# Kernel optimization log

Hardware: AMD Instinct MI355X
Metric: run time of the kernel (lower is better)

The kernel has to match this reference:

```python
import jax, jax.numpy as jnp
import numpy as np

B, S, IN, OUT = 4, 2048, 4096, 1024
ROUNDS = 12  # prime_factors(4096) == [2]*12
QMIN, QMAX = -128, 127


def _create_noise(key, shape, lo, hi):
    # Obfuscation noise spanning the data range; exactly corrected in forward.
    return jax.random.uniform(key, shape, jnp.float32, -0.5, 0.5) * (hi - lo)


def setup_inputs() -> dict:
    key = jax.random.key(0)
    ks = jax.random.split(key, 6)
    x = jax.random.normal(ks[0], (B, S, IN), jnp.float32)
    weight = jax.random.normal(ks[1], (OUT, IN), jnp.float32) * 0.02
    bias = jax.random.normal(ks[2], (OUT,), jnp.float32) * 0.02
    weight_noise = _create_noise(ks[3], (OUT, IN), weight.min(), weight.max())
    noise_x = _create_noise(ks[4], (B, S, IN), x.min(), x.max())
    # one random permutation of in_features per round
    perms = jnp.stack([jax.random.permutation(jax.random.fold_in(key, 1000 + r), IN)
                       for r in range(ROUNDS)]).astype(jnp.int32)
    # 2048 random orthogonal 2x2 blocks per round (rotations, like ortho_group with dim=2)
    theta = jax.random.uniform(ks[5], (ROUNDS, IN // 2), jnp.float32, 0.0, 2.0 * np.pi)
    c, s = jnp.cos(theta), jnp.sin(theta)
    row0 = jnp.stack([c, -s], axis=-1)
    row1 = jnp.stack([s, c], axis=-1)
    matrices = jnp.stack([row0, row1], axis=-2)  # (ROUNDS, IN//2, 2, 2)
    return {"x": x, "weight": weight, "bias": bias, "weight_noise": weight_noise,
            "noise_x": noise_x, "permutations": perms, "matrices": matrices}


def _permute_matrix_operation(X, perms, mats):
    # X: (..., n, cols). Each round: gather rows by permutation, then apply a
    # block-diagonal orthogonal transform (G blocks of size f along the n axis).
    lead = X.shape[:-2]
    n, cols = X.shape[-2], X.shape[-1]
    G, f = mats.shape[1], mats.shape[2]
    for r in range(mats.shape[0]):
        X = jnp.take(X, perms[r], axis=-2)
        Xb = X.reshape(lead + (G, f, cols))
        X = jnp.einsum('gij,...gjc->...gic', mats[r], Xb).reshape(lead + (n, cols))
    return X


def _quant_dequant(t):
    # Asymmetric per-tensor quantize -> round -> clamp -> dequantize (int8-style).
    lo, hi = t.min(), t.max()
    scale = (hi - lo) / (QMAX - QMIN)
    zp = jnp.round(QMIN - lo / scale)
    q = jnp.clip(jnp.round(t / scale + zp), QMIN, QMAX)
    return (q - zp) * scale


def reference(x, weight, bias, weight_noise, noise_x, permutations, matrices):
    # inverse-transpose blocks; equals `matrices` for orthogonal blocks, kept explicit for fidelity
    inv_mats_mT = jnp.swapaxes(jnp.linalg.inv(matrices), -1, -2)
    w_plus = weight + weight_noise                                   # (OUT, IN)
    permuted_w = jnp.swapaxes(
        _permute_matrix_operation(jnp.swapaxes(w_plus, -1, -2), permutations, inv_mats_mT), -1, -2)
    qw = _quant_dequant(permuted_w)                                  # (OUT, IN)
    permuted_x = jnp.swapaxes(
        _permute_matrix_operation(jnp.swapaxes(x + noise_x, -1, -2), permutations, matrices), -1, -2)
    qx = _quant_dequant(permuted_x)                                  # (B, S, IN)
    res = qx @ qw.T + bias                                           # quantized matmul + bias
    res = res - x @ weight_noise.T                                   # correction term 1
    res = res - noise_x @ w_plus.T                                   # correction term 2
    return res
```

## Files before the change

kernel.cpp:

```cpp
#include <hip/hip_runtime.h>


#define IN_F   4096
#define OUT_F  1024
#define MROWS  8192
#define KTOT   12288
#define NROUNDS 12

typedef _Float16 f16;
typedef _Float16 f16x8 __attribute__((ext_vector_type(8)));
typedef _Float16 f16x4 __attribute__((ext_vector_type(4)));
typedef float    f32x4 __attribute__((ext_vector_type(4)));

#define OFF_XT  (0ull)
#define OFF_WT  (OFF_XT + (size_t)MROWS * IN_F * 4)
#define OFF_A   (OFF_WT + (size_t)OUT_F * IN_F * 4)
#define OFF_B   (OFF_A + (size_t)MROWS * KTOT * 2)
#define OFF_MM  (OFF_B + (size_t)OUT_F * KTOT * 2)

__device__ __forceinline__ unsigned enc_f(float f) {
  unsigned u = __float_as_uint(f);
  return (u & 0x80000000u) ? ~u : (u | 0x80000000u);
}
__device__ __forceinline__ float dec_f(unsigned u) {
  unsigned b = (u & 0x80000000u) ? (u & 0x7fffffffu) : ~u;
  return __uint_as_float(b);
}

__global__ void init_mm_kernel(unsigned* mm) {
  mm[0] = 0xFFFFFFFFu;
  mm[1] = 0u;
  mm[2] = 0xFFFFFFFFu;
  mm[3] = 0u;
}

template <bool IS_W>
__global__ __launch_bounds__(256) void transform_kernel(
    const float* __restrict__ in0, const float* __restrict__ in1,
    const int* __restrict__ perms, const float* __restrict__ mats,
    float* __restrict__ tout, f16* __restrict__ f16out,
    unsigned* __restrict__ mm, int mmidx) {
  __shared__ float2 buf[2][IN_F];
  const int t = threadIdx.x;
  const size_t m0 = (size_t)blockIdx.x * 2;

  const float4* r0a = (const float4*)(in0 + m0 * IN_F);
  const float4* r0b = (const float4*)(in1 + m0 * IN_F);
  const float4* r1a = (const float4*)(in0 + (m0 + 1) * IN_F);
  const float4* r1b = (const float4*)(in1 + (m0 + 1) * IN_F);
  f16* f0 = f16out + m0 * KTOT;
  f16* f1 = f16out + (m0 + 1) * KTOT;

#pragma unroll
  for (int j = 0; j < 4; j++) {
    int i4 = j * 256 + t;
    float4 a0 = r0a[i4], b0 = r0b[i4], a1 = r1a[i4], b1 = r1b[i4];
    float4 s0 = make_float4(a0.x + b0.x, a0.y + b0.y, a0.z + b0.z, a0.w + b0.w);
    float4 s1 = make_float4(a1.x + b1.x, a1.y + b1.y, a1.z + b1.z, a1.w + b1.w);
    int c = i4 * 4;
    *(float4*)&buf[0][c]     = make_float4(s0.x, s1.x, s0.y, s1.y);
    *(float4*)&buf[0][c + 2] = make_float4(s0.z, s1.z, s0.w, s1.w);
    f16x4 p0, p1, q0, q1;
    if (IS_W) {
      p0.x=(f16)b0.x; p0.y=(f16)b0.y; p0.z=(f16)b0.z; p0.w=(f16)b0.w;
      q0.x=(f16)s0.x; q0.y=(f16)s0.y; q0.z=(f16)s0.z; q0.w=(f16)s0.w;
      p1.x=(f16)b1.x; p1.y=(f16)b1.y; p1.z=(f16)b1.z; p1.w=(f16)b1.w;
      q1.x=(f16)s1.x; q1.y=(f16)s1.y; q1.z=(f16)s1.z; q1.w=(f16)s1.w;
    } else {
      p0.x=(f16)(-a0.x); p0.y=(f16)(-a0.y); p0.z=(f16)(-a0.z); p0.w=(f16)(-a0.w);
      q0.x=(f16)(-b0.x); q0.y=(f16)(-b0.y); q0.z=(f16)(-b0.z); q0.w=(f16)(-b0.w);
      p1.x=(f16)(-a1.x); p1.y=(f16)(-a1.y); p1.z=(f16)(-a1.z); p1.w=(f16)(-a1.w);
      q1.x=(f16)(-b1.x); q1.y=(f16)(-b1.y); q1.z=(f16)(-b1.z); q1.w=(f16)(-b1.w);
    }
    *(f16x4*)(f0 + IN_F + c)     = p0;
    *(f16x4*)(f0 + 2 * IN_F + c) = q0;
    *(f16x4*)(f1 + IN_F + c)     = p1;
    *(f16x4*)(f1 + 2 * IN_F + c) = q1;
  }
  __syncthreads();

  int cur = 0;
  for (int r = 0; r < NROUNDS; r++) {
    const int2* prow = (const int2*)(perms + (size_t)r * IN_F);
    const float4* mrow = (const float4*)(mats + (size_t)r * (IN_F / 2) * 4);
#pragma unroll
    for (int i = 0; i < 8; i++) {
      int g = i * 256 + t;
      int2 p = prow[g];
      float4 m = mrow[g];
      float2 X0 = buf[cur][p.x];
      float2 X1 = buf[cur][p.y];
      float y0x, y0y, y1x, y1y;
      if (IS_W) {
        float rd = 1.0f / (m.x * m.w - m.y * m.z);
        y0x = (m.w * X0.x - m.z * X1.x) * rd;
        y0y = (m.w * X0.y - m.z * X1.y) * rd;
        y1x = (m.x * X1.x - m.y * X0.x) * rd;
        y1y = (m.x * X1.y - m.y * X0.y) * rd;
      } else {
        y0x = m.x * X0.x + m.y * X1.x;
        y0y = m.x * X0.y + m.y * X1.y;
        y1x = m.z * X0.x + m.w * X1.x;
        y1y = m.z * X0.y + m.w * X1.y;
      }
      *(float4*)&buf[cur ^ 1][2 * g] = make_float4(y0x, y0y, y1x, y1y);
    }
    cur ^= 1;
    __syncthreads();
  }
  float lmin = 3.4e38f, lmax = -3.4e38f;
  float4* o0 = (float4*)(tout + m0 * IN_F);
  float4* o1 = (float4*)(tout + (m0 + 1) * IN_F);
#pragma unroll
  for (int j = 0; j < 4; j++) {
    int i4 = j * 256 + t;
    int c = i4 * 4;
    float4 q0 = *(float4*)&buf[0][c];
    float4 q1 = *(float4*)&buf[0][c + 2];
    o0[i4] = make_float4(q0.x, q0.z, q1.x, q1.z);
    o1[i4] = make_float4(q0.y, q0.w, q1.y, q1.w);
    lmin = fminf(lmin, fminf(fminf(q0.x, q0.y), fminf(q0.z, q0.w)));
    lmin = fminf(lmin, fminf(fminf(q1.x, q1.y), fminf(q1.z, q1.w)));
    lmax = fmaxf(lmax, fmaxf(fmaxf(q0.x, q0.y), fmaxf(q0.z, q0.w)));
    lmax = fmaxf(lmax, fmaxf(fmaxf(q1.x, q1.y), fmaxf(q1.z, q1.w)));
  }
#pragma unroll
  for (int off = 32; off > 0; off >>= 1) {
    lmin = fminf(lmin, __shfl_down(lmin, off));
    lmax = fmaxf(lmax, __shfl_down(lmax, off));
  }
  float* red = (float*)&buf[1][0];
  int wid = t >> 6;
  if ((t & 63) == 0) { red[wid * 2] = lmin; red[wid * 2 + 1] = lmax; }
  __syncthreads();
  if (t == 0) {
    float bmin = fminf(fminf(red[0], red[2]), fminf(red[4], red[6]));
    float bmax = fmaxf(fmaxf(red[1], red[3]), fmaxf(red[5], red[7]));
    atomicMin(&mm[mmidx], enc_f(bmin));
    atomicMax(&mm[mmidx + 1], enc_f(bmax));
  }
}

__global__ void finalize_kernel(unsigned* mm) {
  float* sc = (float*)(mm + 4);
  float xlo = dec_f(mm[0]), xhi = dec_f(mm[1]);
  float wlo = dec_f(mm[2]), whi = dec_f(mm[3]);
  float sx = (xhi - xlo) / 255.0f;
  float zx = rintf(-128.0f - xlo / sx);
  float sw = (whi - wlo) / 255.0f;
  float zw = rintf(-128.0f - wlo / sw);
  sc[0] = sx; sc[1] = zx; sc[2] = sw; sc[3] = zw;
}

__global__ __launch_bounds__(256) void quant_kernel(
    const float* __restrict__ src, f16* __restrict__ dst,
    const unsigned* __restrict__ mm, int scoff) {
  const float* sc = (const float*)(mm + 4);
  float s = sc[scoff], zp = sc[scoff + 1];
  int m = blockIdx.x, t = threadIdx.x;
  const float4* srow = (const float4*)(src + (size_t)m * IN_F);
  f16* drow = dst + (size_t)m * KTOT;
#pragma unroll
  for (int j = 0; j < 4; j++) {
    int i4 = j * 256 + t;
    float4 v = srow[i4];
    float q0 = (fminf(fmaxf(rintf(v.x / s + zp), -128.f), 127.f) - zp) * s;
    float q1 = (fminf(fmaxf(rintf(v.y / s + zp), -128.f), 127.f) - zp) * s;
    float q2 = (fminf(fmaxf(rintf(v.z / s + zp), -128.f), 127.f) - zp) * s;
    float q3 = (fminf(fmaxf(rintf(v.w / s + zp), -128.f), 127.f) - zp) * s;
    f16x4 o; o.x = (f16)q0; o.y = (f16)q1; o.z = (f16)q2; o.w = (f16)q3;
    *(f16x4*)(drow + i4 * 4) = o;
  }
}

__device__ __forceinline__ void gl2lds16(const void* g, void* l) {
  __builtin_amdgcn_global_load_lds(
      (__attribute__((address_space(1))) void*)g,
      (__attribute__((address_space(3))) void*)l, 16, 0, 0);
}

__global__ __launch_bounds__(256, 2) void gemm_kernel(
    const f16* __restrict__ A, const f16* __restrict__ B,
    const float* __restrict__ bias, float* __restrict__ out) {
  __shared__ f16 As[128 * 32];
  __shared__ f16 Bs[128 * 32];
  const int tid = threadIdx.x;
  const int wave = tid >> 6, lane = tid & 63;
  const int quad = lane >> 4, fr = lane & 15;
  const int bm = blockIdx.x >> 3, bn = blockIdx.x & 7;
  const int wm = (wave & 1) * 64, wn = (wave >> 1) * 64;

  f32x4 acc[4][4] = {};

  const int l4 = lane >> 2;
  const int lc = (lane & 3) * 8;
  const size_t arow = (size_t)(bm * 128 + wave * 16 + l4);
  const size_t brow = (size_t)(bn * 128 + wave * 16 + l4);
  const f16* ag0 = A + arow * KTOT + lc;
  const f16* ag1 = A + (arow + 64) * KTOT + lc;
  const f16* bg0 = B + brow * KTOT + lc;
  const f16* bg1 = B + (brow + 64) * KTOT + lc;
  f16* as0 = As + (wave * 16) * 32;
  f16* as1 = As + (64 + wave * 16) * 32;
  f16* bs0 = Bs + (wave * 16) * 32;
  f16* bs1 = Bs + (64 + wave * 16) * 32;

  for (int kk = 0; kk < KTOT; kk += 32) {
    gl2lds16(ag0 + kk, as0);
    gl2lds16(ag1 + kk, as1);
    gl2lds16(bg0 + kk, bs0);
    gl2lds16(bg1 + kk, bs1);
    __syncthreads();
    f16x8 af[4], bf[4];
#pragma unroll
    for (int mi = 0; mi < 4; mi++)
      af[mi] = *(const f16x8*)(As + (wm + mi * 16 + fr) * 32 + quad * 8);
#pragma unroll
    for (int ni = 0; ni < 4; ni++)
      bf[ni] = *(const f16x8*)(Bs + (wn + ni * 16 + fr) * 32 + quad * 8);
#pragma unroll
    for (int mi = 0; mi < 4; mi++)
#pragma unroll
      for (int ni = 0; ni < 4; ni++)
        acc[mi][ni] = __builtin_amdgcn_mfma_f32_16x16x32_f16(
            af[mi], bf[ni], acc[mi][ni], 0, 0, 0);
    __syncthreads();
  }

#pragma unroll
  for (int mi = 0; mi < 4; mi++) {
    int gm = bm * 128 + wm + mi * 16 + quad * 4;
#pragma unroll
    for (int ni = 0; ni < 4; ni++) {
      int gn = bn * 128 + wn + ni * 16 + fr;
      float bv = bias[gn];
#pragma unroll
      for (int e = 0; e < 4; e++)
        out[(size_t)(gm + e) * OUT_F + gn] = acc[mi][ni][e] + bv;
    }
  }
}

extern "C" void kernel_launch(void* const* d_in, const int* in_sizes, int n_in,
                              void* d_out, int out_size, void* d_ws, size_t ws_size,
                              hipStream_t stream) {
  const float* x     = (const float*)d_in[0];
  const float* w     = (const float*)d_in[1];
  const float* bias  = (const float*)d_in[2];
  const float* wn    = (const float*)d_in[3];
  const float* nx    = (const float*)d_in[4];
  const int*   perms = (const int*)d_in[5];
  const float* mats  = (const float*)d_in[6];
  float* out = (float*)d_out;

  char* ws = (char*)d_ws;
  float* xt   = (float*)(ws + OFF_XT);
  float* wt   = (float*)(ws + OFF_WT);
  f16*   Aall = (f16*)(ws + OFF_A);
  f16*   Ball = (f16*)(ws + OFF_B);
  unsigned* mm = (unsigned*)(ws + OFF_MM);

  init_mm_kernel<<<1, 1, 0, stream>>>(mm);
  transform_kernel<false><<<MROWS / 2, 256, 0, stream>>>(x, nx, perms, mats, xt, Aall, mm, 0);
  transform_kernel<true><<<OUT_F / 2, 256, 0, stream>>>(w, wn, perms, mats, wt, Ball, mm, 2);
  finalize_kernel<<<1, 1, 0, stream>>>(mm);
  quant_kernel<<<MROWS, 256, 0, stream>>>(xt, Aall, mm, 0);
  quant_kernel<<<OUT_F, 256, 0, stream>>>(wt, Ball, mm, 2);
  gemm_kernel<<<(MROWS / 128) * (OUT_F / 128), 256, 0, stream>>>(Aall, Ball, bias, out);
}
```

Measured before the change: 821.7 us.

## Fuse pairs of permute-rotate rounds into precomputed 4-tap tables

A small kernel precomputes, for each pair of rounds, composed gather indices and combined 2x4 coefficients, including the inverse-transpose for the weight path. The transform kernel then runs 6 passes instead of 12, halving LDS round-trips and barriers at the cost of 4 gathers per output pair instead of 2. The GEMM block mapping is also changed so consecutive blocks walk along M for a fixed N tile, changing L2 reuse of the B operand. The fused coefficients are computed in fp32, so rounding differs slightly from the sequential rounds.

```diff
diff --git a/kernel.cpp b/kernel.cpp
--- a/kernel.cpp
+++ b/kernel.cpp
@@ -6,6 +6,7 @@
 #define MROWS  8192
 #define KTOT   12288
 #define NROUNDS 12
+#define NPASS  6
 
 typedef _Float16 f16;
 typedef _Float16 f16x8 __attribute__((ext_vector_type(8)));
@@ -17,6 +18,10 @@
 #define OFF_A   (OFF_WT + (size_t)OUT_F * IN_F * 4)
 #define OFF_B   (OFF_A + (size_t)MROWS * KTOT * 2)
 #define OFF_MM  (OFF_B + (size_t)OUT_F * KTOT * 2)
+#define OFF_TIX (OFF_MM + 256)
+#define OFF_TCX (OFF_TIX + (size_t)NPASS * 2048 * 16)
+#define OFF_TIW (OFF_TCX + (size_t)NPASS * 2048 * 32)
+#define OFF_TCW (OFF_TIW + (size_t)NPASS * 2048 * 16)
 
 __device__ __forceinline__ unsigned enc_f(float f) {
   unsigned u = __float_as_uint(f);
@@ -34,10 +39,50 @@
   mm[3] = 0u;
 }
 
+__global__ void build_tables_kernel(const int* __restrict__ perms,
+                                    const float* __restrict__ mats,
+                                    int4* __restrict__ tIx, float4* __restrict__ tCx,
+                                    int4* __restrict__ tIw, float4* __restrict__ tCw) {
+  int p = blockIdx.x;
+  int r0 = 2 * p, r1 = 2 * p + 1;
+  for (int g = threadIdx.x; g < 2048; g += blockDim.x) {
+    int q0 = perms[r1 * IN_F + 2 * g], q1 = perms[r1 * IN_F + 2 * g + 1];
+    int a0 = q0 >> 1, e0 = q0 & 1, a1 = q1 >> 1, e1 = q1 & 1;
+    int4 idx = make_int4(perms[r0 * IN_F + 2 * a0], perms[r0 * IN_F + 2 * a0 + 1],
+                         perms[r0 * IN_F + 2 * a1], perms[r0 * IN_F + 2 * a1 + 1]);
+    const float* Ma = mats + ((size_t)r0 * 2048 + a0) * 4;
+    const float* Mb = mats + ((size_t)r0 * 2048 + a1) * 4;
+    const float* M1 = mats + ((size_t)r1 * 2048 + g) * 4;
+    int o = p * 2048 + g;
+    {
+      float c00 = Ma[e0 * 2], c01 = Ma[e0 * 2 + 1];
+      float c10 = Mb[e1 * 2], c11 = Mb[e1 * 2 + 1];
+      float m00 = M1[0], m01 = M1[1], m10 = M1[2], m11 = M1[3];
+      tIx[o] = idx;
+      tCx[2 * o]     = make_float4(m00 * c00, m00 * c01, m01 * c10, m01 * c11);
+      tCx[2 * o + 1] = make_float4(m10 * c00, m10 * c01, m11 * c10, m11 * c11);
+    }
+    {
+      float rda = 1.0f / (Ma[0] * Ma[3] - Ma[1] * Ma[2]);
+      float rdb = 1.0f / (Mb[0] * Mb[3] - Mb[1] * Mb[2]);
+      float rd1 = 1.0f / (M1[0] * M1[3] - M1[1] * M1[2]);
+      float c00 = (e0 == 0 ? Ma[3] : -Ma[1]) * rda;
+      float c01 = (e0 == 0 ? -Ma[2] : Ma[0]) * rda;
+      float c10 = (e1 == 0 ? Mb[3] : -Mb[1]) * rdb;
+      float c11 = (e1 == 0 ? -Mb[2] : Mb[0]) * rdb;
+      float m00 = M1[3] * rd1, m01 = -M1[2] * rd1;
+      float m10 = -M1[1] * rd1, m11 = M1[0] * rd1;
+      tIw[o] = idx;
+      tCw[2 * o]     = make_float4(m00 * c00, m00 * c01, m01 * c10, m01 * c11);
+      tCw[2 * o + 1] = make_float4(m10 * c00, m10 * c01, m11 * c10, m11 * c11);
+    }
+  }
+}
+
 template <bool IS_W>
 __global__ __launch_bounds__(256) void transform_kernel(
     const float* __restrict__ in0, const float* __restrict__ in1,
-    const int* __restrict__ perms, const float* __restrict__ mats,
+    const int4* __restrict__ tI, const float4* __restrict__ tC,
     float* __restrict__ tout, f16* __restrict__ f16out,
     unsigned* __restrict__ mm, int mmidx) {
   __shared__ float2 buf[2][IN_F];
@@ -80,29 +125,20 @@
   __syncthreads();
 
   int cur = 0;
-  for (int r = 0; r < NROUNDS; r++) {
-    const int2* prow = (const int2*)(perms + (size_t)r * IN_F);
-    const float4* mrow = (const float4*)(mats + (size_t)r * (IN_F / 2) * 4);
+  for (int pass = 0; pass < NPASS; pass++) {
+    const int4* ti = tI + pass * 2048;
+    const float4* tc = tC + (size_t)pass * 4096;
 #pragma unroll
     for (int i = 0; i < 8; i++) {
       int g = i * 256 + t;
-      int2 p = prow[g];
-      float4 m = mrow[g];
-      float2 X0 = buf[cur][p.x];
-      float2 X1 = buf[cur][p.y];
-      float y0x, y0y, y1x, y1y;
-      if (IS_W) {
-        float rd = 1.0f / (m.x * m.w - m.y * m.z);
-        y0x = (m.w * X0.x - m.z * X1.x) * rd;
-        y0y = (m.w * X0.y - m.z * X1.y) * rd;
-        y1x = (m.x * X1.x - m.y * X0.x) * rd;
-        y1y = (m.x * X1.y - m.y * X0.y) * rd;
-      } else {
-        y0x = m.x * X0.x + m.y * X1.x;
-        y0y = m.x * X0.y + m.y * X1.y;
-        y1x = m.z * X0.x + m.w * X1.x;
-        y1y = m.z * X0.y + m.w * X1.y;
-      }
+      int4 id = ti[g];
+      float4 cA = tc[2 * g], cB = tc[2 * g + 1];
+      float2 x0 = buf[cur][id.x], x1 = buf[cur][id.y];
+      float2 x2 = buf[cur][id.z], x3 = buf[cur][id.w];
+      float y0x = cA.x * x0.x + cA.y * x1.x + cA.z * x2.x + cA.w * x3.x;
+      float y0y = cA.x * x0.y + cA.y * x1.y + cA.z * x2.y + cA.w * x3.y;
+      float y1x = cB.x * x0.x + cB.y * x1.x + cB.z * x2.x + cB.w * x3.x;
+      float y1y = cB.x * x0.y + cB.y * x1.y + cB.z * x2.y + cB.w * x3.y;
       *(float4*)&buf[cur ^ 1][2 * g] = make_float4(y0x, y0y, y1x, y1y);
     }
     cur ^= 1;
@@ -187,7 +223,7 @@
   const int tid = threadIdx.x;
   const int wave = tid >> 6, lane = tid & 63;
   const int quad = lane >> 4, fr = lane & 15;
-  const int bm = blockIdx.x >> 3, bn = blockIdx.x & 7;
+  const int bm = blockIdx.x & 63, bn = blockIdx.x >> 6;
   const int wm = (wave & 1) * 64, wn = (wave >> 1) * 64;
 
   f32x4 acc[4][4] = {};
@@ -259,10 +295,15 @@
   f16*   Aall = (f16*)(ws + OFF_A);
   f16*   Ball = (f16*)(ws + OFF_B);
   unsigned* mm = (unsigned*)(ws + OFF_MM);
+  int4*   tIx = (int4*)(ws + OFF_TIX);
+  float4* tCx = (float4*)(ws + OFF_TCX);
+  int4*   tIw = (int4*)(ws + OFF_TIW);
+  float4* tCw = (float4*)(ws + OFF_TCW);
 
   init_mm_kernel<<<1, 1, 0, stream>>>(mm);
-  transform_kernel<false><<<MROWS / 2, 256, 0, stream>>>(x, nx, perms, mats, xt, Aall, mm, 0);
-  transform_kernel<true><<<OUT_F / 2, 256, 0, stream>>>(w, wn, perms, mats, wt, Ball, mm, 2);
+  build_tables_kernel<<<NPASS, 256, 0, stream>>>(perms, mats, tIx, tCx, tIw, tCw);
+  transform_kernel<false><<<MROWS / 2, 256, 0, stream>>>(x, nx, tIx, tCx, xt, Aall, mm, 0);
+  transform_kernel<true><<<OUT_F / 2, 256, 0, stream>>>(w, wn, tIw, tCw, wt, Ball, mm, 2);
   finalize_kernel<<<1, 1, 0, stream>>>(mm);
   quant_kernel<<<MROWS, 256, 0, stream>>>(xt, Aall, mm, 0);
   quant_kernel<<<OUT_F, 256, 0, stream>>>(wt, Ball, mm, 2);
```

Result: faster. 755.4 us (-8.1%).
